# Kernel optimization log

Hardware: AMD Instinct MI355X
Metric: run time of the kernel (lower is better)

## Reference

```python
import jax, jax.numpy as jnp
import numpy as np

INNER_DIM = 128
GRU_DIM = 256
HAN_DIM = 512  # hidden_size_HANLayer * num_heads_HANLayer = 64 * 8
B = 32
N = 8192


def setup_inputs() -> dict:
    key = jax.random.key(0)
    k1, k2, k3, k4, k5 = jax.random.split(key, 5)
    change_embeddings = jax.random.normal(k1, (B, N, GRU_DIM), dtype=jnp.float32)
    edges_embeddings = jax.random.normal(k2, (N, HAN_DIM), dtype=jnp.float32)
    mask = jax.random.randint(k3, (B, N), 0, 2) == 1
    # nn.Linear weights: [out_features, in_features], no bias
    Wq = jax.random.normal(k4, (INNER_DIM, GRU_DIM), dtype=jnp.float32) * (GRU_DIM ** -0.5)
    Wk = jax.random.normal(k5, (INNER_DIM, HAN_DIM), dtype=jnp.float32) * (HAN_DIM ** -0.5)
    return {"change_embeddings": change_embeddings, "edges_embeddings": edges_embeddings,
            "mask": mask, "Wq": Wq, "Wk": Wk}


def reference(change_embeddings, edges_embeddings, mask, Wq, Wk):
    # k: [n, inner]
    k = edges_embeddings @ Wk.T
    # q: [B, n, inner]  (per-batch projection of change embeddings)
    q = jnp.einsum('bnd,ed->bne', change_embeddings, Wq)
    # Original computes full [n,n] q@k^T per batch then takes diag; that is just
    # the row-wise dot product q[b,j] . k[j], computed directly here.
    sim = jnp.einsum('bne,ne->bn', q, k) * (INNER_DIM ** -0.5)  # [B, n]
    mask_sim = jnp.where(mask, sim, jnp.float32(-1e9))
    out = jax.nn.softmax(mask_sim, axis=0)  # softmax over the batch dim
    return out.T  # [n, B]
```

## Files before the change

### kernel.cpp

```cpp
#include <hip/hip_runtime.h>

#define NTOK 8192
#define BDIM 32
#define GRU  256
#define HAN  512
#define INNER 128
static constexpr float SCALE = 0.08838834764831845f;

__global__ __launch_bounds__(256) void make_m(const float* __restrict__ Wk,
                                              const float* __restrict__ Wq,
                                              const void* __restrict__ maskp,
                                              float* __restrict__ M,
                                              int* __restrict__ flag) {
    const int e = blockIdx.x;
    const int j = threadIdx.x;
    float acc = 0.0f;
#pragma unroll 8
    for (int i = 0; i < INNER; ++i)
        acc = fmaf(Wk[(size_t)i * HAN + e], Wq[(size_t)i * GRU + j], acc);
    M[(size_t)e * GRU + j] = SCALE * acc;

    if (e == 0 && j < 64) {
        const unsigned int* mi = (const unsigned int*)maskp;
        const int ok = __all((int)(mi[j] <= 1u)) ? 1 : 0;
        if (j == 0) *flag = ok;
    }
}

__global__ __launch_bounds__(256) void gemm_tile(const float* __restrict__ A,
                                                 const float* __restrict__ B,
                                                 float* __restrict__ C,
                                                 int M, int K, int J) {
    __shared__ float As[32][68];
    __shared__ float Bs[32][68];

    const int t  = threadIdx.x;
    const int n0 = blockIdx.x * 64;
    const int j0 = blockIdx.y * 64;
    const int tn = t >> 4;
    const int tj = t & 15;

    const int r_l = t >> 2;
    const int kq  = t & 3;
    const int k_l = t >> 4;
    const int j4  = (t & 15) * 4;

    float acc[4][4];
#pragma unroll
    for (int i = 0; i < 4; ++i)
#pragma unroll
        for (int j = 0; j < 4; ++j) acc[i][j] = 0.0f;

    for (int kc = 0; kc < K; kc += 32) {
#pragma unroll
        for (int h = 0; h < 2; ++h) {
            const int kb = kq * 4 + h * 16;
            const float4 a = *(const float4*)(A + (size_t)(n0 + r_l) * K + kc + kb);
            As[kb + 0][r_l] = a.x;
            As[kb + 1][r_l] = a.y;
            As[kb + 2][r_l] = a.z;
            As[kb + 3][r_l] = a.w;
        }
#pragma unroll
        for (int h = 0; h < 2; ++h) {
            const int kr = k_l + h * 16;
            *(float4*)&Bs[kr][j4] =
                *(const float4*)(B + (size_t)(kc + kr) * J + j0 + j4);
        }
        __syncthreads();

#pragma unroll
        for (int kk = 0; kk < 32; ++kk) {
            const float4 a4 = *(const float4*)&As[kk][tn * 4];
            const float4 b4 = *(const float4*)&Bs[kk][tj * 4];
            const float av[4] = {a4.x, a4.y, a4.z, a4.w};
            const float bv[4] = {b4.x, b4.y, b4.z, b4.w};
#pragma unroll
            for (int i = 0; i < 4; ++i)
#pragma unroll
                for (int j = 0; j < 4; ++j)
                    acc[i][j] = fmaf(av[i], bv[j], acc[i][j]);
        }
        __syncthreads();
    }

#pragma unroll
    for (int i = 0; i < 4; ++i) {
        float4 o;
        o.x = acc[i][0];
        o.y = acc[i][1];
        o.z = acc[i][2];
        o.w = acc[i][3];
        *(float4*)(C + (size_t)(n0 + tn * 4 + i) * J + j0 + tj * 4) = o;
    }
}

__global__ __launch_bounds__(512) void cal_sim_main(const float* __restrict__ chg,
                                                    const void* __restrict__ maskp,
                                                    const float* __restrict__ w,
                                                    const int* __restrict__ flag,
                                                    float* __restrict__ out) {
    __shared__ float sim[BDIM][17];
    __shared__ float mrow[16], srow[16];

    const int t  = threadIdx.x;
    const int n0 = blockIdx.x * 16;

    const int wave = t >> 6;
    const int half = (t >> 5) & 1;
    const int dq   = t & 31;
    const int nloc = wave * 2 + half;
    const int n    = n0 + nloc;

    const float4 wr0 = *(const float4*)(w + (size_t)n * GRU + dq * 8);
    const float4 wr1 = *(const float4*)(w + (size_t)n * GRU + dq * 8 + 4);

    const int misi = *flag;
    const int* mi = (const int*)maskp;
    const unsigned char* mb = (const unsigned char*)maskp;

#pragma unroll 8
    for (int b = 0; b < BDIM; ++b) {
        const float* cp = chg + ((size_t)b * NTOK + n) * GRU + dq * 8;
        const float4 c0 = *(const float4*)(cp);
        const float4 c1 = *(const float4*)(cp + 4);
        float p;
        p = c0.x * wr0.x;
        p = fmaf(c0.y, wr0.y, p);
        p = fmaf(c0.z, wr0.z, p);
        p = fmaf(c0.w, wr0.w, p);
        p = fmaf(c1.x, wr1.x, p);
        p = fmaf(c1.y, wr1.y, p);
        p = fmaf(c1.z, wr1.z, p);
        p = fmaf(c1.w, wr1.w, p);
        p += __shfl_xor(p, 1, 64);
        p += __shfl_xor(p, 2, 64);
        p += __shfl_xor(p, 4, 64);
        p += __shfl_xor(p, 8, 64);
        p += __shfl_xor(p, 16, 64);
        if (dq == 0) {
            const size_t mofs = (size_t)b * NTOK + n;
            const int mval = misi ? mi[mofs] : (int)mb[mofs];
            sim[b][nloc] = mval ? p : -1e9f;
        }
    }
    __syncthreads();

    if (t < 16) {
        float m = sim[0][t];
        for (int b = 1; b < BDIM; ++b) m = fmaxf(m, sim[b][t]);
        float s = 0.0f;
        for (int b = 0; b < BDIM; ++b) s += __expf(sim[b][t] - m);
        mrow[t] = m;
        srow[t] = 1.0f / s;
    }
    __syncthreads();

    {
        const int b  = t & 31;
        const int nl = t >> 5;
        out[(size_t)n0 * BDIM + t] = __expf(sim[b][nl] - mrow[nl]) * srow[nl];
    }
}

extern "C" void kernel_launch(void* const* d_in, const int* in_sizes, int n_in,
                              void* d_out, int out_size, void* d_ws, size_t ws_size,
                              hipStream_t stream) {
    const float* chg   = (const float*)d_in[0];
    const float* edges = (const float*)d_in[1];
    const void*  mask  = d_in[2];
    const float* Wq    = (const float*)d_in[3];
    const float* Wk    = (const float*)d_in[4];
    float* out = (float*)d_out;

    float* wws  = (float*)d_ws;
    float* Mws  = wws + (size_t)NTOK * GRU;
    int*   flag = (int*)(Mws + (size_t)HAN * GRU);

    make_m<<<HAN, 256, 0, stream>>>(Wk, Wq, mask, Mws, flag);

    gemm_tile<<<dim3(NTOK / 64, GRU / 64), 256, 0, stream>>>(
        edges, Mws, wws, NTOK, HAN, GRU);

    cal_sim_main<<<NTOK / 16, 512, 0, stream>>>(chg, mask, wws, flag, out);
}
```

Baseline: 408.1 us.

## Fuse edges-by-M projection into the similarity kernel via LDS

Drops the separate tiled GEMM that wrote the projected edge matrix w (8192x256) to global memory. Each similarity block now computes its own 16 rows of w in shared memory straight from the edge embeddings and M, then reads them from LDS. This saves one launch and a global write plus read of w. In exchange every block streams all of M (512x256) from L2/global without LDS tiling, so reuse is lower and each block has a longer serial GEMM phase before the bandwidth-bound reduction over the change embeddings.

Result: slower. 550.6 us (+34.9%).

```diff
diff --git a/kernel.cpp b/kernel.cpp
--- a/kernel.cpp
+++ b/kernel.cpp
@@ -27,84 +27,64 @@
     }
 }
 
-__global__ __launch_bounds__(256) void gemm_tile(const float* __restrict__ A,
-                                                 const float* __restrict__ B,
-                                                 float* __restrict__ C,
-                                                 int M, int K, int J) {
-    __shared__ float As[32][68];
-    __shared__ float Bs[32][68];
-
-    const int t  = threadIdx.x;
-    const int n0 = blockIdx.x * 64;
-    const int j0 = blockIdx.y * 64;
-    const int tn = t >> 4;
-    const int tj = t & 15;
-
-    const int r_l = t >> 2;
-    const int kq  = t & 3;
-    const int k_l = t >> 4;
-    const int j4  = (t & 15) * 4;
-
-    float acc[4][4];
-#pragma unroll
-    for (int i = 0; i < 4; ++i)
-#pragma unroll
-        for (int j = 0; j < 4; ++j) acc[i][j] = 0.0f;
-
-    for (int kc = 0; kc < K; kc += 32) {
-#pragma unroll
-        for (int h = 0; h < 2; ++h) {
-            const int kb = kq * 4 + h * 16;
-            const float4 a = *(const float4*)(A + (size_t)(n0 + r_l) * K + kc + kb);
-            As[kb + 0][r_l] = a.x;
-            As[kb + 1][r_l] = a.y;
-            As[kb + 2][r_l] = a.z;
-            As[kb + 3][r_l] = a.w;
-        }
-#pragma unroll
-        for (int h = 0; h < 2; ++h) {
-            const int kr = k_l + h * 16;
-            *(float4*)&Bs[kr][j4] =
-                *(const float4*)(B + (size_t)(kc + kr) * J + j0 + j4);
-        }
-        __syncthreads();
-
-#pragma unroll
-        for (int kk = 0; kk < 32; ++kk) {
-            const float4 a4 = *(const float4*)&As[kk][tn * 4];
-            const float4 b4 = *(const float4*)&Bs[kk][tj * 4];
-            const float av[4] = {a4.x, a4.y, a4.z, a4.w};
-            const float bv[4] = {b4.x, b4.y, b4.z, b4.w};
-#pragma unroll
-            for (int i = 0; i < 4; ++i)
-#pragma unroll
-                for (int j = 0; j < 4; ++j)
-                    acc[i][j] = fmaf(av[i], bv[j], acc[i][j]);
-        }
-        __syncthreads();
-    }
-
-#pragma unroll
-    for (int i = 0; i < 4; ++i) {
-        float4 o;
-        o.x = acc[i][0];
-        o.y = acc[i][1];
-        o.z = acc[i][2];
-        o.w = acc[i][3];
-        *(float4*)(C + (size_t)(n0 + tn * 4 + i) * J + j0 + tj * 4) = o;
-    }
-}
-
-__global__ __launch_bounds__(512) void cal_sim_main(const float* __restrict__ chg,
-                                                    const void* __restrict__ maskp,
-                                                    const float* __restrict__ w,
-                                                    const int* __restrict__ flag,
-                                                    float* __restrict__ out) {
+__global__ __launch_bounds__(512) void cal_sim_fused(const float* __restrict__ chg,
+                                                     const float* __restrict__ edges,
+                                                     const void* __restrict__ maskp,
+                                                     const float* __restrict__ M,
+                                                     const int* __restrict__ flag,
+                                                     float* __restrict__ out) {
+    __shared__ float w_lds[16][GRU];
     __shared__ float sim[BDIM][17];
     __shared__ float mrow[16], srow[16];
 
     const int t  = threadIdx.x;
     const int n0 = blockIdx.x * 16;
+
+    {
+        const int tg = t & 7;
+        const int jg = t >> 3;
+        const int j0 = jg * 4;
+        const int na = tg * 2;
+        const int nb = na + 1;
+
+        const float* ea_p = edges + (size_t)(n0 + na) * HAN;
+        const float* eb_p = edges + (size_t)(n0 + nb) * HAN;
+
+        float acc0[4] = {0.f, 0.f, 0.f, 0.f};
+        float acc1[4] = {0.f, 0.f, 0.f, 0.f};
+
+        for (int ec = 0; ec < HAN; ec += 16) {
+            float4 ea[4], eb[4];
+#pragma unroll
+            for (int q = 0; q < 4; ++q) {
+                ea[q] = *(const float4*)(ea_p + ec + q * 4);
+                eb[q] = *(const float4*)(eb_p + ec + q * 4);
+            }
+#pragma unroll
+            for (int q = 0; q < 4; ++q) {
+                const float eav[4] = {ea[q].x, ea[q].y, ea[q].z, ea[q].w};
+                const float ebv[4] = {eb[q].x, eb[q].y, eb[q].z, eb[q].w};
+#pragma unroll
+                for (int el = 0; el < 4; ++el) {
+                    const float4 m4 =
+                        *(const float4*)(M + (size_t)(ec + q * 4 + el) * GRU + j0);
+                    const float va = eav[el];
+                    const float vb = ebv[el];
+                    acc0[0] = fmaf(va, m4.x, acc0[0]);
+                    acc0[1] = fmaf(va, m4.y, acc0[1]);
+                    acc0[2] = fmaf(va, m4.z, acc0[2]);
+                    acc0[3] = fmaf(va, m4.w, acc0[3]);
+                    acc1[0] = fmaf(vb, m4.x, acc1[0]);
+                    acc1[1] = fmaf(vb, m4.y, acc1[1]);
+                    acc1[2] = fmaf(vb, m4.z, acc1[2]);
+                    acc1[3] = fmaf(vb, m4.w, acc1[3]);
+                }
+            }
+        }
+        *(float4*)&w_lds[na][j0] = make_float4(acc0[0], acc0[1], acc0[2], acc0[3]);
+        *(float4*)&w_lds[nb][j0] = make_float4(acc1[0], acc1[1], acc1[2], acc1[3]);
+    }
+    __syncthreads();
 
     const int wave = t >> 6;
     const int half = (t >> 5) & 1;
@@ -112,8 +92,8 @@
     const int nloc = wave * 2 + half;
     const int n    = n0 + nloc;
 
-    const float4 wr0 = *(const float4*)(w + (size_t)n * GRU + dq * 8);
-    const float4 wr1 = *(const float4*)(w + (size_t)n * GRU + dq * 8 + 4);
+    const float4 wr0 = *(const float4*)&w_lds[nloc][dq * 8];
+    const float4 wr1 = *(const float4*)&w_lds[nloc][dq * 8 + 4];
 
     const int misi = *flag;
     const int* mi = (const int*)maskp;
@@ -173,14 +153,10 @@
     const float* Wk    = (const float*)d_in[4];
     float* out = (float*)d_out;
 
-    float* wws  = (float*)d_ws;
-    float* Mws  = wws + (size_t)NTOK * GRU;
+    float* Mws  = (float*)d_ws;
     int*   flag = (int*)(Mws + (size_t)HAN * GRU);
 
     make_m<<<HAN, 256, 0, stream>>>(Wk, Wq, mask, Mws, flag);
 
-    gemm_tile<<<dim3(NTOK / 64, GRU / 64), 256, 0, stream>>>(
-        edges, Mws, wws, NTOK, HAN, GRU);
-
-    cal_sim_main<<<NTOK / 16, 512, 0, stream>>>(chg, mask, wws, flag, out);
+    cal_sim_fused<<<NTOK / 16, 512, 0, stream>>>(chg, edges, mask, Mws, flag, out);
 }
```
